# Performance work log

Measured on AMD Instinct MI355X. Metric: run time of the kernel, lower is better.

Reference implementation:

```python
import jax, jax.numpy as jnp
import numpy as np

B, N, F_IN, H1, H2 = 32, 1024, 512, 256, 128


def _leaky(x, alpha):
    return jnp.where(x >= 0, x, alpha * x)


def _gat_layer(x, W, a, alpha=0.01, concat=True):
    # x: [B,N,Fin], W: [Fin,Fout], a: [2*Fout,1]
    h = x @ W                              # [B,N,Fout]
    Fo = W.shape[1]
    # The repeat+cat+matmul(a) in torch is exactly a_left . h_i + a_right . h_j
    el = h @ a[:Fo, 0]                     # [B,N]
    er = h @ a[Fo:, 0]                     # [B,N]
    e = _leaky(el[:, :, None] + er[:, None, :], alpha)   # [B,N,N]
    # global per-batch min-max normalization, then *30 - 20
    mn = jnp.min(e, axis=(1, 2), keepdims=True)
    mx = jnp.max(e, axis=(1, 2), keepdims=True)
    e = (e - mn) / (mx - mn) * 30.0 - 20.0
    att = jax.nn.sigmoid(e)                # [B,N,N]; dropout is a no-op in eval
    hp = att @ h                           # [B,N,Fout]
    if concat:
        hp = jax.nn.elu(hp)
    return hp, att


def setup_inputs() -> dict:
    key = jax.random.key(0)
    ks = jax.random.split(key, 8)
    x = jax.random.normal(ks[0], (B, N, F_IN), dtype=jnp.float32)
    edge_weight = jax.random.normal(ks[1], (B, N, N), dtype=jnp.float32)
    def xavier(k, shape):
        fan_in, fan_out = shape[0], shape[1]
        lim = 1.414 * np.sqrt(6.0 / (fan_in + fan_out))
        return jax.random.uniform(k, shape, jnp.float32, -lim, lim)
    W1 = xavier(ks[2], (F_IN, H1))
    a1 = xavier(ks[3], (2 * H1, 1))
    W2 = xavier(ks[4], (H1, H2))
    a2 = xavier(ks[5], (2 * H2, 1))
    Wg = jax.random.normal(ks[6], (H2, 1), dtype=jnp.float32) * np.sqrt(2.0 / H2)
    bg = jnp.zeros((1,), dtype=jnp.float32)
    return {"x": x, "edge_weight": edge_weight, "W1": W1, "a1": a1,
            "W2": W2, "a2": a2, "Wg": Wg, "bg": bg}


def reference(x, edge_weight, W1, a1, W2, a2, Wg, bg):
    # edge_weight ('adj') is never used inside GraphAttentionLayer.forward
    g1, fc1 = _gat_layer(x, W1, a1, alpha=0.01, concat=True)
    g2, fc2 = _gat_layer(g1, W2, a2, alpha=0.01, concat=False)
    # VanillaGCN: leaky_relu(BN(Linear(adj @ feats))); BN is identity in eval
    z = (fc2 @ g2) @ Wg + bg               # [B,N,1]
    out = _leaky(z, 0.01)
    return out, fc2, g2
```

## Files before the change

### kernel.cpp

```cpp
#include <hip/hip_runtime.h>

#define NN 1024
#define FIN 512
#define HH1 256
#define HH2 128
#define MTOT 32768

typedef unsigned short ushort_t;
using bf16x8 = __attribute__((ext_vector_type(8))) short;
using f32x4  = __attribute__((ext_vector_type(4))) float;

__device__ __forceinline__ float leakyf(float x) { return fmaxf(x, 0.01f * x); }
__device__ __forceinline__ float eluf(float x) { return x > 0.0f ? x : __expf(x) - 1.0f; }
__device__ __forceinline__ unsigned pack_hi(unsigned u0, unsigned u1) {
  return __builtin_amdgcn_perm(u1, u0, 0x07060302u);
}
__device__ __forceinline__ void split_pack2(float f0, float f1, unsigned& hp, unsigned& lp) {
  unsigned u0 = __float_as_uint(f0), u1 = __float_as_uint(f1);
  hp = pack_hi(u0, u1);
  float l0 = f0 - __uint_as_float(u0 & 0xFFFF0000u);
  float l1 = f1 - __uint_as_float(u1 & 0xFFFF0000u);
  lp = pack_hi(__float_as_uint(l0), __float_as_uint(l1));
}
__device__ __forceinline__ unsigned pack_rne(float f0, float f1) {
  unsigned u0 = __float_as_uint(f0); u0 += 0x7FFFu + ((u0 >> 16) & 1u);
  unsigned u1 = __float_as_uint(f1); u1 += 0x7FFFu + ((u1 >> 16) & 1u);
  return pack_hi(u0, u1);
}

__global__ __launch_bounds__(256) void transpose_w_split(const float* __restrict__ W,
                                                         ushort_t* __restrict__ WThi,
                                                         ushort_t* __restrict__ WTlo,
                                                         int Nc, int kshift) {
  int idx = blockIdx.x * 256 + threadIdx.x;
  int k = idx & ((1 << kshift) - 1);
  int n = idx >> kshift;
  float f = W[(size_t)k * Nc + n];
  unsigned u = __float_as_uint(f);
  WThi[idx] = (ushort_t)(u >> 16);
  float lo = f - __uint_as_float(u & 0xFFFF0000u);
  WTlo[idx] = (ushort_t)(__float_as_uint(lo) >> 16);
}

template<int NC, int NCB>
__global__ __launch_bounds__(256, 4) void gemm_asplit(const float* __restrict__ A,
                                                      const ushort_t* __restrict__ BThi,
                                                      const ushort_t* __restrict__ BTlo,
                                                      const float* __restrict__ avec,
                                                      ushort_t* __restrict__ CThi,
                                                      ushort_t* __restrict__ CTlo,
                                                      float* __restrict__ el,
                                                      float* __restrict__ er, int K) {
  constexpr int NFR = NCB / 32;
  constexpr int NB  = NCB / 64;
  __shared__ ushort_t Ah[64 * 40], Al[64 * 40];
  __shared__ ushort_t Bbuf[NCB * 80];
  __shared__ float aL[NCB], aR[NCB];
  ushort_t* Bh = Bbuf;
  ushort_t* Bl = Bbuf + NCB * 40;
  const int t = threadIdx.x, lane = t & 63, wid = t >> 6;
  const int wm = (wid & 1) * 32, wn = (wid >> 1) * (NCB / 2);
  const int ln = lane & 15, quad = lane >> 4;
  const int m0 = blockIdx.x * 64;
  const int n0c = blockIdx.y * NCB;
  if (t < NCB) { aL[t] = avec[n0c + t]; aR[t] = avec[NC + n0c + t]; }
  const int ra = t >> 2, ka = (t & 3) * 8;
  const float* ap = A + (size_t)(m0 + ra) * K + ka;
  const int brow = (t >> 2);
  const int bko  = (t & 3) * 8;
  f32x4 acc[2][NFR];
#pragma unroll
  for (int mi = 0; mi < 2; ++mi)
#pragma unroll
    for (int ni = 0; ni < NFR; ++ni) acc[mi][ni] = (f32x4){0.f, 0.f, 0.f, 0.f};

  for (int k0 = 0; k0 < K; k0 += 32) {
    float4 fa0 = *(const float4*)(ap + k0);
    float4 fa1 = *(const float4*)(ap + k0 + 4);
    uint4 vbh[NB], vbl[NB];
#pragma unroll
    for (int i = 0; i < NB; ++i) {
      size_t off = (size_t)(n0c + brow + i * 64) * K + k0 + bko;
      vbh[i] = *(const uint4*)&BThi[off];
      vbl[i] = *(const uint4*)&BTlo[off];
    }
    uint4 ah4, al4;
    split_pack2(fa0.x, fa0.y, ah4.x, al4.x);
    split_pack2(fa0.z, fa0.w, ah4.y, al4.y);
    split_pack2(fa1.x, fa1.y, ah4.z, al4.z);
    split_pack2(fa1.z, fa1.w, ah4.w, al4.w);
    __syncthreads();
    *(uint4*)&Ah[ra * 40 + ka] = ah4;
    *(uint4*)&Al[ra * 40 + ka] = al4;
#pragma unroll
    for (int i = 0; i < NB; ++i) {
      *(uint4*)&Bh[(brow + i * 64) * 40 + bko] = vbh[i];
      *(uint4*)&Bl[(brow + i * 64) * 40 + bko] = vbl[i];
    }
    __syncthreads();
    bf16x8 ahf[2], alf[2], bhf[NFR], blf[NFR];
#pragma unroll
    for (int i = 0; i < 2; ++i) {
      const int ao = (wm + i * 16 + ln) * 40 + quad * 8;
      ahf[i] = *(const bf16x8*)&Ah[ao];
      alf[i] = *(const bf16x8*)&Al[ao];
    }
#pragma unroll
    for (int i = 0; i < NFR; ++i) {
      const int bo = (wn + i * 16 + ln) * 40 + quad * 8;
      bhf[i] = *(const bf16x8*)&Bh[bo];
      blf[i] = *(const bf16x8*)&Bl[bo];
    }
#pragma unroll
    for (int mi = 0; mi < 2; ++mi)
#pragma unroll
      for (int ni = 0; ni < NFR; ++ni) {
        acc[mi][ni] = __builtin_amdgcn_mfma_f32_16x16x32_bf16(ahf[mi], bhf[ni], acc[mi][ni], 0, 0, 0);
        acc[mi][ni] = __builtin_amdgcn_mfma_f32_16x16x32_bf16(ahf[mi], blf[ni], acc[mi][ni], 0, 0, 0);
        acc[mi][ni] = __builtin_amdgcn_mfma_f32_16x16x32_bf16(alf[mi], bhf[ni], acc[mi][ni], 0, 0, 0);
      }
  }

#pragma unroll
  for (int mi = 0; mi < 2; ++mi) {
    const int mr = m0 + wm + mi * 16 + quad * 4;
#pragma unroll
    for (int rr = 0; rr < 4; ++rr) {
      float vel = 0.f, ver = 0.f;
#pragma unroll
      for (int ni = 0; ni < NFR; ++ni) {
        const int c = wn + ni * 16 + ln;
        vel = fmaf(acc[mi][ni][rr], aL[c], vel);
        ver = fmaf(acc[mi][ni][rr], aR[c], ver);
      }
#pragma unroll
      for (int m = 1; m < 16; m <<= 1) {
        vel += __shfl_xor(vel, m);
        ver += __shfl_xor(ver, m);
      }
      if (ln == 0) {
        atomicAdd(&el[mr + rr], vel);
        atomicAdd(&er[mr + rr], ver);
      }
    }
  }

  ushort_t* dsthi = CThi + (size_t)blockIdx.x * (NC * 64) + (size_t)n0c * 64;
  ushort_t* dstlo = CTlo + (size_t)blockIdx.x * (NC * 64) + (size_t)n0c * 64;
  const int colbase = wid * (NCB / 4);
  const int g = lane >> 2, j = lane & 3;
#pragma unroll
  for (int pass = 0; pass < 2; ++pass) {
    __syncthreads();
#pragma unroll
    for (int mi = 0; mi < 2; ++mi) {
      const int rbase = wm + mi * 16 + quad * 4;
#pragma unroll
      for (int ni = 0; ni < NFR; ++ni) {
        const int c = wn + ni * 16 + ln;
        unsigned h01, l01, h23, l23;
        split_pack2(acc[mi][ni][0], acc[mi][ni][1], h01, l01);
        split_pack2(acc[mi][ni][2], acc[mi][ni][3], h23, l23);
        uint2 v = pass ? make_uint2(l01, l23) : make_uint2(h01, h23);
        *(uint2*)&Bbuf[c * 66 + rbase] = v;
      }
    }
    __syncthreads();
    ushort_t* dst = pass ? dstlo : dsthi;
#pragma unroll
    for (int cc = 0; cc < NCB / 64; ++cc) {
      const int col = colbase + cc * 16 + g;
#pragma unroll
      for (int half = 0; half < 2; ++half) {
        const int r = half * 32 + j * 8;
        *(uint4*)&dst[col * 64 + r] = *(const uint4*)&Bbuf[col * 66 + r];
      }
    }
  }
}

__global__ __launch_bounds__(256) void minmax_params(const float* __restrict__ el,
                                                     const float* __restrict__ er,
                                                     float2* __restrict__ params) {
  __shared__ float smnl[256], smxl[256], smnr[256], smxr[256];
  const int b = blockIdx.x, t = threadIdx.x;
  float mnl = 3.4e38f, mxl = -3.4e38f, mnr = 3.4e38f, mxr = -3.4e38f;
  for (int i = t; i < NN; i += 256) {
    float v = el[b * NN + i];
    mnl = fminf(mnl, v); mxl = fmaxf(mxl, v);
    float u = er[b * NN + i];
    mnr = fminf(mnr, u); mxr = fmaxf(mxr, u);
  }
  smnl[t] = mnl; smxl[t] = mxl; smnr[t] = mnr; smxr[t] = mxr;
  __syncthreads();
  for (int s = 128; s > 0; s >>= 1) {
    if (t < s) {
      smnl[t] = fminf(smnl[t], smnl[t + s]);
      smxl[t] = fmaxf(smxl[t], smxl[t + s]);
      smnr[t] = fminf(smnr[t], smnr[t + s]);
      smxr[t] = fmaxf(smxr[t], smxr[t + s]);
    }
    __syncthreads();
  }
  if (t == 0) {
    float mn = leakyf(smnl[0] + smnr[0]);
    float mx = leakyf(smxl[0] + smxr[0]);
    params[b] = make_float2(mn, 30.0f / (mx - mn));
  }
}

template<int BW>
__global__ __launch_bounds__(256, 4) void gemm_att2(const float* __restrict__ el,
                                                    const float* __restrict__ er,
                                                    const float2* __restrict__ params,
                                                    const ushort_t* __restrict__ hThi,
                                                    const ushort_t* __restrict__ hTlo,
                                                    float* __restrict__ C,
                                                    const float* __restrict__ wg,
                                                    float* __restrict__ wv,
                                                    int Nc, int doElu) {
  constexpr int NFR = BW / 32;
  __shared__ ushort_t Ah[64 * 40];
  __shared__ ushort_t Bh[BW * 40], Bl[BW * 40];
  __shared__ float ers[NN];
  __shared__ float wls[BW];
  const int b = blockIdx.z, t = threadIdx.x, lane = t & 63, wid = t >> 6;
  const int wm = (wid & 1) * 32, wn = (wid >> 1) * (BW / 2);
  const int ln = lane & 15, quad = lane >> 4;
  const int m0 = blockIdx.x * 64, n0 = blockIdx.y * BW;
  const float2 p = params[b];
  const float npinv = -p.y;
  const float npc   = p.x * p.y + 20.0f;
  *(float4*)&ers[t * 4] = *(const float4*)&er[b * NN + t * 4];
  if (wg && t < BW) wls[t] = wg[n0 + t];
  const int ra = t >> 2, ka = (t & 3) * 8;
  const float elv = el[b * NN + m0 + ra];
  const int rb = (BW == 128) ? (t >> 1) : (t >> 2);
  const int kb = (BW == 128) ? ((t & 1) * 16) : ((t & 3) * 8);
  const size_t tstride = (size_t)Nc * 64;
  const size_t rowoff  = (size_t)(n0 + rb) * 64 + kb;
  f32x4 acc[2][NFR];
#pragma unroll
  for (int mi = 0; mi < 2; ++mi)
#pragma unroll
    for (int ni = 0; ni < NFR; ++ni) acc[mi][ni] = (f32x4){0.f, 0.f, 0.f, 0.f};
  __syncthreads();

  for (int k0 = 0; k0 < NN; k0 += 32) {
    const size_t toff = (size_t)(b * 16 + (k0 >> 6)) * tstride + (size_t)(k0 & 32) + rowoff;
    uint4 vbh0 = *(const uint4*)&hThi[toff];
    uint4 vbl0 = *(const uint4*)&hTlo[toff];
    uint4 vbh1, vbl1;
    if constexpr (BW == 128) {
      vbh1 = *(const uint4*)&hThi[toff + 8];
      vbl1 = *(const uint4*)&hTlo[toff + 8];
    }
    float s[8];
#pragma unroll
    for (int j = 0; j < 8; ++j) {
      float x = elv + ers[k0 + ka + j];
      x = fmaxf(x, 0.01f * x);
      s[j] = __builtin_amdgcn_rcpf(1.0f + __expf(fmaf(x, npinv, npc)));
    }
    uint4 av;
    av.x = pack_rne(s[0], s[1]); av.y = pack_rne(s[2], s[3]);
    av.z = pack_rne(s[4], s[5]); av.w = pack_rne(s[6], s[7]);
    __syncthreads();
    *(uint4*)&Ah[ra * 40 + ka] = av;
    *(uint4*)&Bh[rb * 40 + kb] = vbh0;
    *(uint4*)&Bl[rb * 40 + kb] = vbl0;
    if constexpr (BW == 128) {
      *(uint4*)&Bh[rb * 40 + kb + 8] = vbh1;
      *(uint4*)&Bl[rb * 40 + kb + 8] = vbl1;
    }
    __syncthreads();
    bf16x8 af[2], bhf[NFR], blf[NFR];
#pragma unroll
    for (int i = 0; i < 2; ++i) af[i] = *(const bf16x8*)&Ah[(wm + i * 16 + ln) * 40 + quad * 8];
#pragma unroll
    for (int i = 0; i < NFR; ++i) {
      const int bo = (wn + i * 16 + ln) * 40 + quad * 8;
      bhf[i] = *(const bf16x8*)&Bh[bo];
      blf[i] = *(const bf16x8*)&Bl[bo];
    }
#pragma unroll
    for (int mi = 0; mi < 2; ++mi)
#pragma unroll
      for (int ni = 0; ni < NFR; ++ni) {
        acc[mi][ni] = __builtin_amdgcn_mfma_f32_16x16x32_bf16(af[mi], bhf[ni], acc[mi][ni], 0, 0, 0);
        acc[mi][ni] = __builtin_amdgcn_mfma_f32_16x16x32_bf16(af[mi], blf[ni], acc[mi][ni], 0, 0, 0);
      }
  }
#pragma unroll
  for (int mi = 0; mi < 2; ++mi) {
    const int mrl = m0 + wm + mi * 16 + quad * 4;
    const size_t mrow = (size_t)b * NN + mrl;
#pragma unroll
    for (int ni = 0; ni < NFR; ++ni) {
      const int c = n0 + wn + ni * 16 + ln;
#pragma unroll
      for (int rr = 0; rr < 4; ++rr) {
        float v = acc[mi][ni][rr];
        if (doElu) v = eluf(v);
        C[(mrow + rr) * Nc + c] = v;
      }
    }
    if (wg) {
#pragma unroll
      for (int rr = 0; rr < 4; ++rr) {
        float vw = 0.f;
#pragma unroll
        for (int ni = 0; ni < NFR; ++ni)
          vw = fmaf(acc[mi][ni][rr], wls[wn + ni * 16 + ln], vw);
#pragma unroll
        for (int m = 1; m < 16; m <<= 1) vw += __shfl_xor(vw, m);
        if (ln == 0) atomicAdd(&wv[b * NN + mrl + rr], vw);
      }
    }
  }
}

__global__ __launch_bounds__(256) void final_out_fc2(const float* __restrict__ el,
                                                     const float* __restrict__ er,
                                                     const float2* __restrict__ params,
                                                     const float* __restrict__ w,
                                                     const float* __restrict__ bg,
                                                     float* __restrict__ fc2,
                                                     float* __restrict__ out) {
  const int row  = (blockIdx.x * 256 + threadIdx.x) >> 6;
  const int lane = threadIdx.x & 63;
  const int b = row >> 10;
  const float2 p = params[b];
  const float npinv = -p.y;
  const float npc   = p.x * p.y + 20.0f;
  const float eli = el[row];
  const float* erb = er + (b << 10);
  const float* wb  = w + (b << 10);
  float* fcrow = fc2 + (size_t)row * NN;
  float s = 0.f;
  for (int j = lane * 4; j < NN; j += 256) {
    float4 e4 = *(const float4*)&erb[j];
    float4 w4 = *(const float4*)&wb[j];
    float4 a;
    a.x = __builtin_amdgcn_rcpf(1.0f + __expf(fmaf(leakyf(eli + e4.x), npinv, npc)));
    a.y = __builtin_amdgcn_rcpf(1.0f + __expf(fmaf(leakyf(eli + e4.y), npinv, npc)));
    a.z = __builtin_amdgcn_rcpf(1.0f + __expf(fmaf(leakyf(eli + e4.z), npinv, npc)));
    a.w = __builtin_amdgcn_rcpf(1.0f + __expf(fmaf(leakyf(eli + e4.w), npinv, npc)));
    s += w4.x * a.x + w4.y * a.y + w4.z * a.z + w4.w * a.w;
    *(float4*)&fcrow[j] = a;
  }
#pragma unroll
  for (int off = 32; off > 0; off >>= 1) s += __shfl_down(s, off);
  if (lane == 0) out[row] = leakyf(s + bg[0]);
}

extern "C" void kernel_launch(void* const* d_in, const int* in_sizes, int n_in,
                              void* d_out, int out_size, void* d_ws, size_t ws_size,
                              hipStream_t stream) {
  (void)in_sizes; (void)n_in; (void)out_size; (void)ws_size;
  const float* x  = (const float*)d_in[0];
  const float* W1 = (const float*)d_in[2];
  const float* a1 = (const float*)d_in[3];
  const float* W2 = (const float*)d_in[4];
  const float* a2 = (const float*)d_in[5];
  const float* Wg = (const float*)d_in[6];
  const float* bg = (const float*)d_in[7];

  float* out = (float*)d_out;
  float* fc2 = out + 32768;
  float* g2  = fc2 + 33554432;

  ushort_t* h1Thi = (ushort_t*)fc2;
  ushort_t* h1Tlo = (ushort_t*)(fc2 + 4194304);
  float*    g1    = fc2 + 8388608;
  ushort_t* h2Thi = (ushort_t*)(fc2 + 16777216);
  ushort_t* h2Tlo = (ushort_t*)(fc2 + 18874368);

  float* wsf = (float*)d_ws;
  float* el1 = wsf;
  float* er1 = wsf + 32768;
  float* el2 = wsf + 65536;
  float* er2 = wsf + 98304;
  float* wv  = wsf + 131072;
  float2* p1 = (float2*)(wsf + 163840);
  float2* p2 = (float2*)(wsf + 163904);
  ushort_t* W1Thi = (ushort_t*)(wsf + 163968);
  ushort_t* W1Tlo = (ushort_t*)(wsf + 229504);
  ushort_t* W2Thi = (ushort_t*)(wsf + 295040);
  ushort_t* W2Tlo = (ushort_t*)(wsf + 311424);

  dim3 blk(256);
  hipMemsetAsync(wsf, 0, 5u * 32768u * sizeof(float), stream);
  transpose_w_split<<<512, blk, 0, stream>>>(W1, W1Thi, W1Tlo, HH1, 9);
  transpose_w_split<<<128, blk, 0, stream>>>(W2, W2Thi, W2Tlo, HH2, 8);
  gemm_asplit<HH1, 128><<<dim3(512, 2), blk, 0, stream>>>(x, W1Thi, W1Tlo, a1,
                                                          h1Thi, h1Tlo, el1, er1, FIN);
  minmax_params<<<32, blk, 0, stream>>>(el1, er1, p1);
  gemm_att2<128><<<dim3(16, 2, 32), blk, 0, stream>>>(el1, er1, p1, h1Thi, h1Tlo,
                                                      g1, nullptr, nullptr, HH1, 1);
  gemm_asplit<HH2, 64><<<dim3(512, 2), blk, 0, stream>>>(g1, W2Thi, W2Tlo, a2,
                                                         h2Thi, h2Tlo, el2, er2, HH1);
  minmax_params<<<32, blk, 0, stream>>>(el2, er2, p2);
  gemm_att2<64><<<dim3(16, 2, 32), blk, 0, stream>>>(el2, er2, p2, h2Thi, h2Tlo,
                                                     g2, Wg, wv, HH2, 0);
  final_out_fc2<<<8192, blk, 0, stream>>>(el2, er2, p2, wv, bg, fc2, out);
}
```

Measured before the change: 484.8 us.

## Load MFMA fragments directly from global memory, drop LDS staging in GEMMs

Both GEMM kernels now have each wave load its A and B MFMA operand fragments straight from global memory into registers. The shared-memory tiles and the two barriers per k-step are gone, and in the attention GEMM each wave computes its own sigmoid A fragments from er values held in LDS. The aim is to remove LDS round-trips and block-wide synchronisation. The cost is that the waves sharing a block now load the same A and B data redundantly, global accesses become narrower strided rows, and the launch-bounds occupancy hint drops from 4 to 2.

After: 574.9 us. +18.6%, slower.

```diff
diff --git a/kernel.cpp b/kernel.cpp
--- a/kernel.cpp
+++ b/kernel.cpp
@@ -43,7 +43,7 @@
 }
 
 template<int NC, int NCB>
-__global__ __launch_bounds__(256, 4) void gemm_asplit(const float* __restrict__ A,
+__global__ __launch_bounds__(256, 2) void gemm_asplit(const float* __restrict__ A,
                                                       const ushort_t* __restrict__ BThi,
                                                       const ushort_t* __restrict__ BTlo,
                                                       const float* __restrict__ avec,
@@ -52,22 +52,16 @@
                                                       float* __restrict__ el,
                                                       float* __restrict__ er, int K) {
   constexpr int NFR = NCB / 32;
-  constexpr int NB  = NCB / 64;
-  __shared__ ushort_t Ah[64 * 40], Al[64 * 40];
-  __shared__ ushort_t Bbuf[NCB * 80];
-  __shared__ float aL[NCB], aR[NCB];
-  ushort_t* Bh = Bbuf;
-  ushort_t* Bl = Bbuf + NCB * 40;
+  __shared__ ushort_t stg[NCB * 66];
   const int t = threadIdx.x, lane = t & 63, wid = t >> 6;
   const int wm = (wid & 1) * 32, wn = (wid >> 1) * (NCB / 2);
   const int ln = lane & 15, quad = lane >> 4;
   const int m0 = blockIdx.x * 64;
   const int n0c = blockIdx.y * NCB;
-  if (t < NCB) { aL[t] = avec[n0c + t]; aR[t] = avec[NC + n0c + t]; }
-  const int ra = t >> 2, ka = (t & 3) * 8;
-  const float* ap = A + (size_t)(m0 + ra) * K + ka;
-  const int brow = (t >> 2);
-  const int bko  = (t & 3) * 8;
+  const float*    ap0 = A + (size_t)(m0 + wm + ln) * K + quad * 8;
+  const float*    ap1 = ap0 + (size_t)16 * K;
+  const ushort_t* bh0 = BThi + (size_t)(n0c + wn + ln) * K + quad * 8;
+  const ushort_t* bl0 = BTlo + (size_t)(n0c + wn + ln) * K + quad * 8;
   f32x4 acc[2][NFR];
 #pragma unroll
   for (int mi = 0; mi < 2; ++mi)
@@ -75,41 +69,33 @@
     for (int ni = 0; ni < NFR; ++ni) acc[mi][ni] = (f32x4){0.f, 0.f, 0.f, 0.f};
 
   for (int k0 = 0; k0 < K; k0 += 32) {
-    float4 fa0 = *(const float4*)(ap + k0);
-    float4 fa1 = *(const float4*)(ap + k0 + 4);
-    uint4 vbh[NB], vbl[NB];
-#pragma unroll
-    for (int i = 0; i < NB; ++i) {
-      size_t off = (size_t)(n0c + brow + i * 64) * K + k0 + bko;
-      vbh[i] = *(const uint4*)&BThi[off];
-      vbl[i] = *(const uint4*)&BTlo[off];
-    }
-    uint4 ah4, al4;
-    split_pack2(fa0.x, fa0.y, ah4.x, al4.x);
-    split_pack2(fa0.z, fa0.w, ah4.y, al4.y);
-    split_pack2(fa1.x, fa1.y, ah4.z, al4.z);
-    split_pack2(fa1.z, fa1.w, ah4.w, al4.w);
-    __syncthreads();
-    *(uint4*)&Ah[ra * 40 + ka] = ah4;
-    *(uint4*)&Al[ra * 40 + ka] = al4;
-#pragma unroll
-    for (int i = 0; i < NB; ++i) {
-      *(uint4*)&Bh[(brow + i * 64) * 40 + bko] = vbh[i];
-      *(uint4*)&Bl[(brow + i * 64) * 40 + bko] = vbl[i];
-    }
-    __syncthreads();
-    bf16x8 ahf[2], alf[2], bhf[NFR], blf[NFR];
-#pragma unroll
-    for (int i = 0; i < 2; ++i) {
-      const int ao = (wm + i * 16 + ln) * 40 + quad * 8;
-      ahf[i] = *(const bf16x8*)&Ah[ao];
-      alf[i] = *(const bf16x8*)&Al[ao];
-    }
+    bf16x8 ahf[2], alf[2];
+    {
+      float4 f0 = *(const float4*)(ap0 + k0);
+      float4 f1 = *(const float4*)(ap0 + k0 + 4);
+      uint4 hv, lv;
+      split_pack2(f0.x, f0.y, hv.x, lv.x);
+      split_pack2(f0.z, f0.w, hv.y, lv.y);
+      split_pack2(f1.x, f1.y, hv.z, lv.z);
+      split_pack2(f1.z, f1.w, hv.w, lv.w);
+      ahf[0] = *(bf16x8*)&hv; alf[0] = *(bf16x8*)&lv;
+    }
+    {
+      float4 f0 = *(const float4*)(ap1 + k0);
+      float4 f1 = *(const float4*)(ap1 + k0 + 4);
+      uint4 hv, lv;
+      split_pack2(f0.x, f0.y, hv.x, lv.x);
+      split_pack2(f0.z, f0.w, hv.y, lv.y);
+      split_pack2(f1.x, f1.y, hv.z, lv.z);
+      split_pack2(f1.z, f1.w, hv.w, lv.w);
+      ahf[1] = *(bf16x8*)&hv; alf[1] = *(bf16x8*)&lv;
+    }
+    bf16x8 bhf[NFR], blf[NFR];
 #pragma unroll
     for (int i = 0; i < NFR; ++i) {
-      const int bo = (wn + i * 16 + ln) * 40 + quad * 8;
-      bhf[i] = *(const bf16x8*)&Bh[bo];
-      blf[i] = *(const bf16x8*)&Bl[bo];
+      uint4 vh = *(const uint4*)(bh0 + (size_t)i * 16 * K + k0);
+      uint4 vl = *(const uint4*)(bl0 + (size_t)i * 16 * K + k0);
+      bhf[i] = *(bf16x8*)&vh; blf[i] = *(bf16x8*)&vl;
     }
 #pragma unroll
     for (int mi = 0; mi < 2; ++mi)
@@ -121,6 +107,12 @@
       }
   }
 
+  float aLc[NFR], aRc[NFR];
+#pragma unroll
+  for (int ni = 0; ni < NFR; ++ni) {
+    aLc[ni] = avec[n0c + wn + ni * 16 + ln];
+    aRc[ni] = avec[NC + n0c + wn + ni * 16 + ln];
+  }
 #pragma unroll
   for (int mi = 0; mi < 2; ++mi) {
     const int mr = m0 + wm + mi * 16 + quad * 4;
@@ -129,9 +121,8 @@
       float vel = 0.f, ver = 0.f;
 #pragma unroll
       for (int ni = 0; ni < NFR; ++ni) {
-        const int c = wn + ni * 16 + ln;
-        vel = fmaf(acc[mi][ni][rr], aL[c], vel);
-        ver = fmaf(acc[mi][ni][rr], aR[c], ver);
+        vel = fmaf(acc[mi][ni][rr], aLc[ni], vel);
+        ver = fmaf(acc[mi][ni][rr], aRc[ni], ver);
       }
 #pragma unroll
       for (int m = 1; m < 16; m <<= 1) {
@@ -151,7 +142,7 @@
   const int g = lane >> 2, j = lane & 3;
 #pragma unroll
   for (int pass = 0; pass < 2; ++pass) {
-    __syncthreads();
+    if (pass) __syncthreads();
 #pragma unroll
     for (int mi = 0; mi < 2; ++mi) {
       const int rbase = wm + mi * 16 + quad * 4;
@@ -162,7 +153,7 @@
         split_pack2(acc[mi][ni][0], acc[mi][ni][1], h01, l01);
         split_pack2(acc[mi][ni][2], acc[mi][ni][3], h23, l23);
         uint2 v = pass ? make_uint2(l01, l23) : make_uint2(h01, h23);
-        *(uint2*)&Bbuf[c * 66 + rbase] = v;
+        *(uint2*)&stg[c * 66 + rbase] = v;
       }
     }
     __syncthreads();
@@ -173,7 +164,7 @@
 #pragma unroll
       for (int half = 0; half < 2; ++half) {
         const int r = half * 32 + j * 8;
-        *(uint4*)&dst[col * 64 + r] = *(const uint4*)&Bbuf[col * 66 + r];
+        *(uint4*)&dst[col * 64 + r] = *(const uint4*)&stg[col * 66 + r];
       }
     }
   }
@@ -210,7 +201,7 @@
 }
 
 template<int BW>
-__global__ __launch_bounds__(256, 4) void gemm_att2(const float* __restrict__ el,
+__global__ __launch_bounds__(256, 2) void gemm_att2(const float* __restrict__ el,
                                                     const float* __restrict__ er,
                                                     const float2* __restrict__ params,
                                                     const ushort_t* __restrict__ hThi,
@@ -220,10 +211,7 @@
                                                     float* __restrict__ wv,
                                                     int Nc, int doElu) {
   constexpr int NFR = BW / 32;
-  __shared__ ushort_t Ah[64 * 40];
-  __shared__ ushort_t Bh[BW * 40], Bl[BW * 40];
   __shared__ float ers[NN];
-  __shared__ float wls[BW];
   const int b = blockIdx.z, t = threadIdx.x, lane = t & 63, wid = t >> 6;
   const int wm = (wid & 1) * 32, wn = (wid >> 1) * (BW / 2);
   const int ln = lane & 15, quad = lane >> 4;
@@ -232,13 +220,11 @@
   const float npinv = -p.y;
   const float npc   = p.x * p.y + 20.0f;
   *(float4*)&ers[t * 4] = *(const float4*)&er[b * NN + t * 4];
-  if (wg && t < BW) wls[t] = wg[n0 + t];
-  const int ra = t >> 2, ka = (t & 3) * 8;
-  const float elv = el[b * NN + m0 + ra];
-  const int rb = (BW == 128) ? (t >> 1) : (t >> 2);
-  const int kb = (BW == 128) ? ((t & 1) * 16) : ((t & 3) * 8);
+  const float elv0 = el[b * NN + m0 + wm + ln];
+  const float elv1 = el[b * NN + m0 + wm + 16 + ln];
   const size_t tstride = (size_t)Nc * 64;
-  const size_t rowoff  = (size_t)(n0 + rb) * 64 + kb;
+  const ushort_t* bh0 = hThi + (size_t)(b * 16) * tstride + (size_t)(n0 + wn + ln) * 64 + quad * 8;
+  const ushort_t* bl0 = hTlo + (size_t)(b * 16) * tstride + (size_t)(n0 + wn + ln) * 64 + quad * 8;
   f32x4 acc[2][NFR];
 #pragma unroll
   for (int mi = 0; mi < 2; ++mi)
@@ -247,41 +233,32 @@
   __syncthreads();
 
   for (int k0 = 0; k0 < NN; k0 += 32) {
-    const size_t toff = (size_t)(b * 16 + (k0 >> 6)) * tstride + (size_t)(k0 & 32) + rowoff;
-    uint4 vbh0 = *(const uint4*)&hThi[toff];
-    uint4 vbl0 = *(const uint4*)&hTlo[toff];
-    uint4 vbh1, vbl1;
-    if constexpr (BW == 128) {
-      vbh1 = *(const uint4*)&hThi[toff + 8];
-      vbl1 = *(const uint4*)&hTlo[toff + 8];
-    }
-    float s[8];
-#pragma unroll
-    for (int j = 0; j < 8; ++j) {
-      float x = elv + ers[k0 + ka + j];
-      x = fmaxf(x, 0.01f * x);
-      s[j] = __builtin_amdgcn_rcpf(1.0f + __expf(fmaf(x, npinv, npc)));
-    }
-    uint4 av;
-    av.x = pack_rne(s[0], s[1]); av.y = pack_rne(s[2], s[3]);
-    av.z = pack_rne(s[4], s[5]); av.w = pack_rne(s[6], s[7]);
-    __syncthreads();
-    *(uint4*)&Ah[ra * 40 + ka] = av;
-    *(uint4*)&Bh[rb * 40 + kb] = vbh0;
-    *(uint4*)&Bl[rb * 40 + kb] = vbl0;
-    if constexpr (BW == 128) {
-      *(uint4*)&Bh[rb * 40 + kb + 8] = vbh1;
-      *(uint4*)&Bl[rb * 40 + kb + 8] = vbl1;
-    }
-    __syncthreads();
-    bf16x8 af[2], bhf[NFR], blf[NFR];
-#pragma unroll
-    for (int i = 0; i < 2; ++i) af[i] = *(const bf16x8*)&Ah[(wm + i * 16 + ln) * 40 + quad * 8];
+    float e8[8];
+    *(float4*)&e8[0] = *(const float4*)&ers[k0 + quad * 8];
+    *(float4*)&e8[4] = *(const float4*)&ers[k0 + quad * 8 + 4];
+    bf16x8 af[2];
+#pragma unroll
+    for (int mi = 0; mi < 2; ++mi) {
+      const float elv = mi ? elv1 : elv0;
+      float s[8];
+#pragma unroll
+      for (int j = 0; j < 8; ++j) {
+        float x = elv + e8[j];
+        x = fmaxf(x, 0.01f * x);
+        s[j] = __builtin_amdgcn_rcpf(1.0f + __expf(fmaf(x, npinv, npc)));
+      }
+      uint4 av;
+      av.x = pack_rne(s[0], s[1]); av.y = pack_rne(s[2], s[3]);
+      av.z = pack_rne(s[4], s[5]); av.w = pack_rne(s[6], s[7]);
+      af[mi] = *(bf16x8*)&av;
+    }
+    const size_t ko = (size_t)(k0 >> 6) * tstride + (size_t)(k0 & 32);
+    bf16x8 bhf[NFR], blf[NFR];
 #pragma unroll
     for (int i = 0; i < NFR; ++i) {
-      const int bo = (wn + i * 16 + ln) * 40 + quad * 8;
-      bhf[i] = *(const bf16x8*)&Bh[bo];
-      blf[i] = *(const bf16x8*)&Bl[bo];
+      uint4 vh = *(const uint4*)(bh0 + ko + i * (16 * 64));
+      uint4 vl = *(const uint4*)(bl0 + ko + i * (16 * 64));
+      bhf[i] = *(bf16x8*)&vh; blf[i] = *(bf16x8*)&vl;
     }
 #pragma unroll
     for (int mi = 0; mi < 2; ++mi)
@@ -290,6 +267,11 @@
         acc[mi][ni] = __builtin_amdgcn_mfma_f32_16x16x32_bf16(af[mi], bhf[ni], acc[mi][ni], 0, 0, 0);
         acc[mi][ni] = __builtin_amdgcn_mfma_f32_16x16x32_bf16(af[mi], blf[ni], acc[mi][ni], 0, 0, 0);
       }
+  }
+  float wgl[NFR];
+  if (wg) {
+#pragma unroll
+    for (int ni = 0; ni < NFR; ++ni) wgl[ni] = wg[n0 + wn + ni * 16 + ln];
   }
 #pragma unroll
   for (int mi = 0; mi < 2; ++mi) {
@@ -311,7 +293,7 @@
         float vw = 0.f;
 #pragma unroll
         for (int ni = 0; ni < NFR; ++ni)
-          vw = fmaf(acc[mi][ni][rr], wls[wn + ni * 16 + ln], vw);
+          vw = fmaf(acc[mi][ni][rr], wgl[ni], vw);
 #pragma unroll
         for (int m = 1; m < 16; m <<= 1) vw += __shfl_xor(vw, m);
         if (ln == 0) atomicAdd(&wv[b * NN + mrl + rr], vw);
```
